# Kernel tuning notes

Measured on AMD Instinct MI355X. Metric: run time of the kernel, lower is better.

The kernel has to match this reference:

```python
import jax, jax.numpy as jnp
import numpy as np

IN_F, OUT_F = 4096, 4096
IN_Q, OUT_Q = IN_F // 4, OUT_F // 4


def setup_inputs() -> dict:
    key = jax.random.key(0)
    kx, kr, ki, kj, kk = jax.random.split(key, 5)
    std = 1.0 / np.sqrt(IN_F)
    x = jax.random.normal(kx, (4, 2048, IN_F), dtype=jnp.float32)
    Wr = std * jax.random.normal(kr, (OUT_Q, IN_Q), dtype=jnp.float32)
    Wi = std * jax.random.normal(ki, (OUT_Q, IN_Q), dtype=jnp.float32)
    Wj = std * jax.random.normal(kj, (OUT_Q, IN_Q), dtype=jnp.float32)
    Wk = std * jax.random.normal(kk, (OUT_Q, IN_Q), dtype=jnp.float32)
    bias = jnp.zeros((OUT_F,), dtype=jnp.float32)
    return {"x": x, "Wr": Wr, "Wi": Wi, "Wj": Wj, "Wk": Wk, "bias": bias}


def _hamilton_block(Wr, Wi, Wj, Wk):
    # Assemble the structured [4*out_q, 4*in_q] Hamilton block weight so the
    # whole op is ONE large GEMM instead of 16 small ones (same math).
    row_r = jnp.concatenate([Wr, -Wi, -Wj, -Wk], axis=1)
    row_i = jnp.concatenate([Wi,  Wr,  Wk, -Wj], axis=1)
    row_j = jnp.concatenate([Wj, -Wk,  Wr,  Wi], axis=1)
    row_k = jnp.concatenate([Wk,  Wj, -Wi,  Wr], axis=1)
    return jnp.concatenate([row_r, row_i, row_j, row_k], axis=0)  # [OUT_F, IN_F]


def reference(x, Wr, Wi, Wj, Wk, bias):
    W = _hamilton_block(Wr, Wi, Wj, Wk)
    # x: [B, S, IN_F] @ W.T -> [B, S, OUT_F]
    out = jnp.einsum('bsf,of->bso', x, W) + bias
    return out
```

## Files before the change

kernel.cpp:

```cpp
#include <hip/hip_runtime.h>
#include <hip/hip_bf16.h>


#define M_DIM 8192
#define N_DIM 4096
#define K_DIM 4096
#define BK 64
#define NT (K_DIM / BK)

typedef __attribute__((ext_vector_type(8))) short bf16x8;
typedef __attribute__((ext_vector_type(4))) float f32x4;
typedef __attribute__((ext_vector_type(8))) unsigned short ushort8;

static __device__ __forceinline__ unsigned short f2bf(float f) {
    unsigned int u = __float_as_uint(f);
    return (unsigned short)((u + 0x7fffu + ((u >> 16) & 1u)) >> 16);
}
static __device__ __forceinline__ unsigned short f2bf_sgn(float f, unsigned int sg) {
    unsigned int u = __float_as_uint(f) ^ sg;
    return (unsigned short)((u + 0x7fffu + ((u >> 16) & 1u)) >> 16);
}

__global__ __launch_bounds__(256) void cvt_x_kernel(const float* __restrict__ x,
                                                    unsigned short* __restrict__ xb) {
    int i = (blockIdx.x * 256 + threadIdx.x) * 8;
    float4 a = *(const float4*)(x + i);
    float4 b = *(const float4*)(x + i + 4);
    ushort8 o;
    o[0] = f2bf(a.x); o[1] = f2bf(a.y); o[2] = f2bf(a.z); o[3] = f2bf(a.w);
    o[4] = f2bf(b.x); o[5] = f2bf(b.y); o[6] = f2bf(b.z); o[7] = f2bf(b.w);
    *(ushort8*)(xb + i) = o;
}

__global__ __launch_bounds__(256) void prep_w_kernel(const float* __restrict__ Wr,
    const float* __restrict__ Wi, const float* __restrict__ Wj,
    const float* __restrict__ Wk, unsigned short* __restrict__ wb) {
    int row = blockIdx.x >> 1;
    int col = ((blockIdx.x & 1) * 256 + threadIdx.x) * 8;
    int p = row >> 10, q = col >> 10;
    int ci = p ^ q;
    const float* src = (ci == 0) ? Wr : (ci == 1) ? Wi : (ci == 2) ? Wj : Wk;
    unsigned int sg = ((0x428Eu >> (p * 4 + q)) & 1u) << 31;
    int so = (row & 1023) * 1024 + (col & 1023);
    float4 a = *(const float4*)(src + so);
    float4 b = *(const float4*)(src + so + 4);
    ushort8 o;
    o[0] = f2bf_sgn(a.x, sg); o[1] = f2bf_sgn(a.y, sg);
    o[2] = f2bf_sgn(a.z, sg); o[3] = f2bf_sgn(a.w, sg);
    o[4] = f2bf_sgn(b.x, sg); o[5] = f2bf_sgn(b.y, sg);
    o[6] = f2bf_sgn(b.z, sg); o[7] = f2bf_sgn(b.w, sg);
    *(ushort8*)(wb + row * 4096 + col) = o;
}

#define GLD16(gp, lp) __builtin_amdgcn_global_load_lds( \
    (const __attribute__((address_space(1))) void*)(gp), \
    (__attribute__((address_space(3))) void*)(lp), 16, 0, 0)

#define BAR()   do { __builtin_amdgcn_s_barrier(); __builtin_amdgcn_sched_barrier(0); } while (0)
#define LGKM0() do { asm volatile("s_waitcnt lgkmcnt(0)" ::: "memory"); \
                     __builtin_amdgcn_sched_barrier(0); } while (0)
#define VM(n)   do { asm volatile("s_waitcnt vmcnt(" #n ")" ::: "memory"); \
                     __builtin_amdgcn_sched_barrier(0); } while (0)

static __device__ __forceinline__ f32x4 MF(bf16x8 a, bf16x8 b, f32x4 c) {
    return __builtin_amdgcn_mfma_f32_16x16x32_bf16(a, b, c, 0, 0, 0);
}

__global__ __launch_bounds__(512, 2) void qgemm_bf16(
    const unsigned short* __restrict__ A, const unsigned short* __restrict__ B,
    const float* __restrict__ bias, float* __restrict__ out)
{
    __shared__ __align__(16) unsigned short Lsh[2][2][2][128 * 64];

    int bid = blockIdx.x;
    int cpx = gridDim.x >> 3;
    int wg  = (bid & 7) * cpx + (bid >> 3);
    int brow = (wg >> 4) * 256;
    int bcol = (wg & 15) * 256;

    int tid   = threadIdx.x;
    int lane  = tid & 63;
    int wid   = tid >> 6;
    int hA    = wid >> 2;
    int nb    = wid & 3;
    int hB    = nb >> 1;
    int rB0   = (nb & 1) << 6;
    int fr    = lane & 15;
    int fslot = lane >> 4;

    const unsigned short* Ag = A + (size_t)brow * K_DIM;
    const unsigned short* Bg = B + (size_t)bcol * K_DIM;

    f32x4 acc[8][4] = {};

    auto stage = [&](int buf, int ab, int half, int t) {
        const unsigned short* g = (ab ? Bg : Ag) + (size_t)(half << 7) * K_DIM + t * BK;
        unsigned short* l = &Lsh[buf][ab][half][0];
        #pragma unroll
        for (int i = 0; i < 2; ++i) {
            int c = i * 512 + tid;
            int r = c >> 3, s = c & 7;
            GLD16(g + (size_t)r * K_DIM + ((s ^ (r & 7)) << 3), l + (c << 3));
        }
    };
    auto rdA = [&](int buf, int mi, int ks) -> bf16x8 {
        int r = mi * 16 + fr;
        int slot = (ks * 4 + fslot) ^ (r & 7);
        return *(const bf16x8*)((const char*)&Lsh[buf][0][hA][0] + r * 128 + (slot << 4));
    };
    auto rdB = [&](int buf, int ni, int ks) -> bf16x8 {
        int r = rB0 + ni * 16 + fr;
        int slot = (ks * 4 + fslot) ^ (r & 7);
        return *(const bf16x8*)((const char*)&Lsh[buf][1][hB][0] + r * 128 + (slot << 4));
    };

    stage(0, 0, 0, 0); stage(0, 0, 1, 0); stage(0, 1, 0, 0); stage(0, 1, 1, 0);
    stage(1, 1, 0, 1); stage(1, 1, 1, 1);
    VM(4); BAR();

    for (int t = 0; t < NT; ++t) {
        int buf = t & 1;
        bf16x8 bfrag[4][2];

        #pragma unroll
        for (int ni = 0; ni < 4; ++ni) {
            bfrag[ni][0] = rdB(buf, ni, 0);
            bfrag[ni][1] = rdB(buf, ni, 1);
        }
        {
            bf16x8 x0 = rdA(buf, 0, 0), x1 = rdA(buf, 0, 1);
            bf16x8 x2 = rdA(buf, 1, 0), x3 = rdA(buf, 1, 1);
            if (t + 1 < NT) stage(buf ^ 1, 0, 0, t + 1);
            BAR(); LGKM0();
            __builtin_amdgcn_s_setprio(1);
            #pragma unroll
            for (int ni = 0; ni < 4; ++ni) {
                acc[0][ni] = MF(x0, bfrag[ni][0], acc[0][ni]);
                acc[0][ni] = MF(x1, bfrag[ni][1], acc[0][ni]);
                acc[1][ni] = MF(x2, bfrag[ni][0], acc[1][ni]);
                acc[1][ni] = MF(x3, bfrag[ni][1], acc[1][ni]);
            }
            __builtin_amdgcn_s_setprio(0);
            BAR();
        }
        {
            bf16x8 x0 = rdA(buf, 2, 0), x1 = rdA(buf, 2, 1);
            bf16x8 x2 = rdA(buf, 3, 0), x3 = rdA(buf, 3, 1);
            if (t + 1 < NT) stage(buf ^ 1, 0, 1, t + 1);
            BAR(); LGKM0();
            __builtin_amdgcn_s_setprio(1);
            #pragma unroll
            for (int ni = 0; ni < 4; ++ni) {
                acc[2][ni] = MF(x0, bfrag[ni][0], acc[2][ni]);
                acc[2][ni] = MF(x1, bfrag[ni][1], acc[2][ni]);
                acc[3][ni] = MF(x2, bfrag[ni][0], acc[3][ni]);
                acc[3][ni] = MF(x3, bfrag[ni][1], acc[3][ni]);
            }
            __builtin_amdgcn_s_setprio(0);
            BAR();
        }
        {
            bf16x8 x0 = rdA(buf, 4, 0), x1 = rdA(buf, 4, 1);
            bf16x8 x2 = rdA(buf, 5, 0), x3 = rdA(buf, 5, 1);
            if (t + 2 < NT) stage(buf, 1, 0, t + 2);
            BAR(); LGKM0();
            __builtin_amdgcn_s_setprio(1);
            #pragma unroll
            for (int ni = 0; ni < 4; ++ni) {
                acc[4][ni] = MF(x0, bfrag[ni][0], acc[4][ni]);
                acc[4][ni] = MF(x1, bfrag[ni][1], acc[4][ni]);
                acc[5][ni] = MF(x2, bfrag[ni][0], acc[5][ni]);
                acc[5][ni] = MF(x3, bfrag[ni][1], acc[5][ni]);
            }
            __builtin_amdgcn_s_setprio(0);
            BAR();
        }
        {
            bf16x8 x0 = rdA(buf, 6, 0), x1 = rdA(buf, 6, 1);
            bf16x8 x2 = rdA(buf, 7, 0), x3 = rdA(buf, 7, 1);
            if (t + 2 < NT) stage(buf, 1, 1, t + 2);
            BAR(); LGKM0();
            __builtin_amdgcn_s_setprio(1);
            #pragma unroll
            for (int ni = 0; ni < 4; ++ni) {
                acc[6][ni] = MF(x0, bfrag[ni][0], acc[6][ni]);
                acc[6][ni] = MF(x1, bfrag[ni][1], acc[6][ni]);
                acc[7][ni] = MF(x2, bfrag[ni][0], acc[7][ni]);
                acc[7][ni] = MF(x3, bfrag[ni][1], acc[7][ni]);
            }
            __builtin_amdgcn_s_setprio(0);
            if (t < NT - 2) { VM(4); } else { VM(0); }
            BAR();
        }
    }

    int cr = (lane >> 4) << 2;
    int cc = lane & 15;
    #pragma unroll
    for (int ni = 0; ni < 4; ++ni) {
        int col = bcol + nb * 64 + ni * 16 + cc;
        float bv = bias[col];
        #pragma unroll
        for (int mi = 0; mi < 8; ++mi) {
            int r0 = brow + hA * 128 + mi * 16 + cr;
            #pragma unroll
            for (int r = 0; r < 4; ++r)
                out[(size_t)(r0 + r) * N_DIM + col] = acc[mi][ni][r] + bv;
        }
    }
}

#define FBM 128
#define FBN 128
#define FBK 64
__global__ __launch_bounds__(256) void qgemm_fb(const float* __restrict__ x,
    const float* __restrict__ Wr, const float* __restrict__ Wi,
    const float* __restrict__ Wj, const float* __restrict__ Wk,
    const float* __restrict__ bias, float* __restrict__ out)
{
    __shared__ unsigned short As[FBM * FBK];
    __shared__ unsigned short Bs[FBN * FBK];

    int bid = blockIdx.x;
    int cpx = gridDim.x >> 3;
    int wg = (bid & 7) * cpx + (bid >> 3);
    int brow = (wg >> 5) * FBM;
    int bcol = (wg & 31) * FBN;

    int tid = threadIdx.x;
    int lane = tid & 63;
    int wv = tid >> 6;
    int wm = (wv >> 1) << 6;
    int wn = (wv & 1) << 6;
    int fr = lane & 15;
    int fk = (lane >> 4) << 3;

    int p = bcol >> 10;
    f32x4 acc[4][4] = {};

    for (int kt = 0; kt < K_DIM / FBK; ++kt) {
        int k0 = kt * FBK;
        int q = k0 >> 10;
        int ci = p ^ q;
        const float* wsrc = (ci == 0) ? Wr : (ci == 1) ? Wi : (ci == 2) ? Wj : Wk;
        unsigned int sg = ((0x428Eu >> (p * 4 + q)) & 1u) << 31;

        __syncthreads();
        #pragma unroll
        for (int i = 0; i < 4; ++i) {
            int c = i * 256 + tid;
            int row = c >> 3, colo = (c & 7) << 3;
            const float* s = x + (size_t)(brow + row) * K_DIM + k0 + colo;
            float4 a = *(const float4*)s;
            float4 b = *(const float4*)(s + 4);
            ushort8 o;
            o[0] = f2bf(a.x); o[1] = f2bf(a.y); o[2] = f2bf(a.z); o[3] = f2bf(a.w);
            o[4] = f2bf(b.x); o[5] = f2bf(b.y); o[6] = f2bf(b.z); o[7] = f2bf(b.w);
            *(ushort8*)(&As[c << 3]) = o;
        }
        #pragma unroll
        for (int i = 0; i < 4; ++i) {
            int c = i * 256 + tid;
            int row = c >> 3, colo = (c & 7) << 3;
            const float* s = wsrc + ((bcol + row) & 1023) * 1024 + ((k0 + colo) & 1023);
            float4 a = *(const float4*)s;
            float4 b = *(const float4*)(s + 4);
            ushort8 o;
            o[0] = f2bf_sgn(a.x, sg); o[1] = f2bf_sgn(a.y, sg);
            o[2] = f2bf_sgn(a.z, sg); o[3] = f2bf_sgn(a.w, sg);
            o[4] = f2bf_sgn(b.x, sg); o[5] = f2bf_sgn(b.y, sg);
            o[6] = f2bf_sgn(b.z, sg); o[7] = f2bf_sgn(b.w, sg);
            *(ushort8*)(&Bs[c << 3]) = o;
        }
        __syncthreads();

        #pragma unroll
        for (int ks = 0; ks < 2; ++ks) {
            bf16x8 af[4], bfr[4];
            #pragma unroll
            for (int m = 0; m < 4; ++m)
                af[m] = *(const bf16x8*)(&As[(wm + m * 16 + fr) * FBK + ks * 32 + fk]);
            #pragma unroll
            for (int n = 0; n < 4; ++n)
                bfr[n] = *(const bf16x8*)(&Bs[(wn + n * 16 + fr) * FBK + ks * 32 + fk]);
            #pragma unroll
            for (int m = 0; m < 4; ++m)
                #pragma unroll
                for (int n = 0; n < 4; ++n)
                    acc[m][n] = __builtin_amdgcn_mfma_f32_16x16x32_bf16(
                        af[m], bfr[n], acc[m][n], 0, 0, 0);
        }
    }

    int cr = (lane >> 4) << 2;
    int cc = lane & 15;
    #pragma unroll
    for (int n = 0; n < 4; ++n) {
        int col = bcol + wn + n * 16 + cc;
        float bv = bias[col];
        #pragma unroll
        for (int m = 0; m < 4; ++m) {
            int r0 = brow + wm + m * 16 + cr;
            #pragma unroll
            for (int r = 0; r < 4; ++r)
                out[(size_t)(r0 + r) * N_DIM + col] = acc[m][n][r] + bv;
        }
    }
}

extern "C" void kernel_launch(void* const* d_in, const int* in_sizes, int n_in,
                              void* d_out, int out_size, void* d_ws, size_t ws_size,
                              hipStream_t stream) {
    const float* x    = (const float*)d_in[0];
    const float* Wr   = (const float*)d_in[1];
    const float* Wi   = (const float*)d_in[2];
    const float* Wj   = (const float*)d_in[3];
    const float* Wk   = (const float*)d_in[4];
    const float* bias = (const float*)d_in[5];
    float* out = (float*)d_out;

    const size_t xb_bytes = (size_t)M_DIM * K_DIM * 2;
    const size_t wb_bytes = (size_t)N_DIM * K_DIM * 2;

    if (ws_size >= xb_bytes + wb_bytes) {
        unsigned short* xb = (unsigned short*)d_ws;
        unsigned short* wb = (unsigned short*)((char*)d_ws + xb_bytes);
        cvt_x_kernel<<<(M_DIM * K_DIM) / 2048, 256, 0, stream>>>(x, xb);
        prep_w_kernel<<<N_DIM * 2, 256, 0, stream>>>(Wr, Wi, Wj, Wk, wb);
        const int n_blocks = (M_DIM / 256) * (N_DIM / 256);
        qgemm_bf16<<<n_blocks, 512, 0, stream>>>(xb, wb, bias, out);
    } else {
        const int n_blocks = (M_DIM / FBM) * (N_DIM / FBN);
        qgemm_fb<<<n_blocks, 256, 0, stream>>>(x, Wr, Wi, Wj, Wk, bias, out);
    }
}
```

Measured before the change: 275.3 us.

## Rebalance prefetch stages, drop explicit LGKM waits and sched barriers, add nontemporal IO

Moves the next-tile A staging into the first sub-phase and shifts the t+2 B stages earlier, leaving the last sub-phase with no global loads. Removes the explicit lgkmcnt(0) waits and the sched_barrier fences so the compiler can interleave LDS reads and MFMAs more freely. Adds nontemporal loads of x in the conversion kernel and nontemporal stores of the output. The risk is that, without the explicit waits, the compiler's own waitcnt insertion and scheduling may reorder things differently, and the earlier staging changes when LDS buffers are overwritten relative to the barriers.

```diff
diff --git a/kernel.cpp b/kernel.cpp
--- a/kernel.cpp
+++ b/kernel.cpp
@@ -24,11 +24,11 @@
 __global__ __launch_bounds__(256) void cvt_x_kernel(const float* __restrict__ x,
                                                     unsigned short* __restrict__ xb) {
     int i = (blockIdx.x * 256 + threadIdx.x) * 8;
-    float4 a = *(const float4*)(x + i);
-    float4 b = *(const float4*)(x + i + 4);
+    f32x4 a = __builtin_nontemporal_load((const f32x4*)(x + i));
+    f32x4 b = __builtin_nontemporal_load((const f32x4*)(x + i + 4));
     ushort8 o;
-    o[0] = f2bf(a.x); o[1] = f2bf(a.y); o[2] = f2bf(a.z); o[3] = f2bf(a.w);
-    o[4] = f2bf(b.x); o[5] = f2bf(b.y); o[6] = f2bf(b.z); o[7] = f2bf(b.w);
+    o[0] = f2bf(a[0]); o[1] = f2bf(a[1]); o[2] = f2bf(a[2]); o[3] = f2bf(a[3]);
+    o[4] = f2bf(b[0]); o[5] = f2bf(b[1]); o[6] = f2bf(b[2]); o[7] = f2bf(b[3]);
     *(ushort8*)(xb + i) = o;
 }
 
@@ -42,13 +42,13 @@
     const float* src = (ci == 0) ? Wr : (ci == 1) ? Wi : (ci == 2) ? Wj : Wk;
     unsigned int sg = ((0x428Eu >> (p * 4 + q)) & 1u) << 31;
     int so = (row & 1023) * 1024 + (col & 1023);
-    float4 a = *(const float4*)(src + so);
-    float4 b = *(const float4*)(src + so + 4);
+    f32x4 a = *(const f32x4*)(src + so);
+    f32x4 b = *(const f32x4*)(src + so + 4);
     ushort8 o;
-    o[0] = f2bf_sgn(a.x, sg); o[1] = f2bf_sgn(a.y, sg);
-    o[2] = f2bf_sgn(a.z, sg); o[3] = f2bf_sgn(a.w, sg);
-    o[4] = f2bf_sgn(b.x, sg); o[5] = f2bf_sgn(b.y, sg);
-    o[6] = f2bf_sgn(b.z, sg); o[7] = f2bf_sgn(b.w, sg);
+    o[0] = f2bf_sgn(a[0], sg); o[1] = f2bf_sgn(a[1], sg);
+    o[2] = f2bf_sgn(a[2], sg); o[3] = f2bf_sgn(a[3], sg);
+    o[4] = f2bf_sgn(b[0], sg); o[5] = f2bf_sgn(b[1], sg);
+    o[6] = f2bf_sgn(b[2], sg); o[7] = f2bf_sgn(b[3], sg);
     *(ushort8*)(wb + row * 4096 + col) = o;
 }
 
@@ -56,11 +56,10 @@
     (const __attribute__((address_space(1))) void*)(gp), \
     (__attribute__((address_space(3))) void*)(lp), 16, 0, 0)
 
-#define BAR()   do { __builtin_amdgcn_s_barrier(); __builtin_amdgcn_sched_barrier(0); } while (0)
-#define LGKM0() do { asm volatile("s_waitcnt lgkmcnt(0)" ::: "memory"); \
-                     __builtin_amdgcn_sched_barrier(0); } while (0)
-#define VM(n)   do { asm volatile("s_waitcnt vmcnt(" #n ")" ::: "memory"); \
-                     __builtin_amdgcn_sched_barrier(0); } while (0)
+#define BAR() do { asm volatile("" ::: "memory"); \
+                   __builtin_amdgcn_s_barrier(); \
+                   asm volatile("" ::: "memory"); } while (0)
+#define VM(n) asm volatile("s_waitcnt vmcnt(" #n ")" ::: "memory")
 
 static __device__ __forceinline__ f32x4 MF(bf16x8 a, bf16x8 b, f32x4 c) {
     return __builtin_amdgcn_mfma_f32_16x16x32_bf16(a, b, c, 0, 0, 0);
@@ -130,8 +129,8 @@
         {
             bf16x8 x0 = rdA(buf, 0, 0), x1 = rdA(buf, 0, 1);
             bf16x8 x2 = rdA(buf, 1, 0), x3 = rdA(buf, 1, 1);
-            if (t + 1 < NT) stage(buf ^ 1, 0, 0, t + 1);
-            BAR(); LGKM0();
+            if (t + 1 < NT) { stage(buf ^ 1, 0, 0, t + 1); stage(buf ^ 1, 0, 1, t + 1); }
+            BAR();
             __builtin_amdgcn_s_setprio(1);
             #pragma unroll
             for (int ni = 0; ni < 4; ++ni) {
@@ -146,8 +145,8 @@
         {
             bf16x8 x0 = rdA(buf, 2, 0), x1 = rdA(buf, 2, 1);
             bf16x8 x2 = rdA(buf, 3, 0), x3 = rdA(buf, 3, 1);
-            if (t + 1 < NT) stage(buf ^ 1, 0, 1, t + 1);
-            BAR(); LGKM0();
+            if (t + 2 < NT) stage(buf, 1, 0, t + 2);
+            BAR();
             __builtin_amdgcn_s_setprio(1);
             #pragma unroll
             for (int ni = 0; ni < 4; ++ni) {
@@ -162,8 +161,8 @@
         {
             bf16x8 x0 = rdA(buf, 4, 0), x1 = rdA(buf, 4, 1);
             bf16x8 x2 = rdA(buf, 5, 0), x3 = rdA(buf, 5, 1);
-            if (t + 2 < NT) stage(buf, 1, 0, t + 2);
-            BAR(); LGKM0();
+            if (t + 2 < NT) stage(buf, 1, 1, t + 2);
+            BAR();
             __builtin_amdgcn_s_setprio(1);
             #pragma unroll
             for (int ni = 0; ni < 4; ++ni) {
@@ -178,8 +177,7 @@
         {
             bf16x8 x0 = rdA(buf, 6, 0), x1 = rdA(buf, 6, 1);
             bf16x8 x2 = rdA(buf, 7, 0), x3 = rdA(buf, 7, 1);
-            if (t + 2 < NT) stage(buf, 1, 1, t + 2);
-            BAR(); LGKM0();
+            BAR();
             __builtin_amdgcn_s_setprio(1);
             #pragma unroll
             for (int ni = 0; ni < 4; ++ni) {
@@ -205,7 +203,8 @@
             int r0 = brow + hA * 128 + mi * 16 + cr;
             #pragma unroll
             for (int r = 0; r < 4; ++r)
-                out[(size_t)(r0 + r) * N_DIM + col] = acc[mi][ni][r] + bv;
+                __builtin_nontemporal_store(acc[mi][ni][r] + bv,
+                                            &out[(size_t)(r0 + r) * N_DIM + col]);
         }
     }
 }
```

New measurement: 274.0 us. Within noise of the previous version (-0.5%).
